# Kernel optimization log

Hardware: AMD Instinct MI355X
Metric: run time of the kernel (lower is better)

Reference implementation:

```python
import jax, jax.numpy as jnp
import numpy as np

B, R, D, H, C = 256, 100, 6168, 128, 100  # batch, replicas, in_dim, hidden, classes


def setup_inputs() -> dict:
    key = jax.random.key(0)
    k1, k2, k3, k4, k5, k6 = jax.random.split(key, 6)
    # binary input features (texas dataset is binary; original casts to bool)
    x = jax.random.randint(k1, (B, D), 0, 2).astype(jnp.int32)
    # Bernoulli(0.5) flip mask, one per replica per feature
    noise = jax.random.randint(k2, (B, R, D), 0, 2).astype(jnp.int32)
    s1 = 1.0 / np.sqrt(D)
    W1 = jax.random.uniform(k3, (D, H), minval=-s1, maxval=s1, dtype=jnp.float32)
    b1 = jax.random.uniform(k4, (H,), minval=-s1, maxval=s1, dtype=jnp.float32)
    s2 = 1.0 / np.sqrt(H)
    W2 = jax.random.uniform(k5, (H, C), minval=-s2, maxval=s2, dtype=jnp.float32)
    b2 = jax.random.uniform(k6, (C,), minval=-s2, maxval=s2, dtype=jnp.float32)
    return {"x": x, "noise": noise, "W1": W1, "b1": b1, "W2": W2, "b2": b2}


def reference(x, noise, W1, b1, W2, b2):
    # np.invert(x, where=noise) on booleans == flip bit where noise==1
    xb = x[:, None, :]                                   # [B,1,D]
    x_noisy = jnp.where(noise == 1, 1 - xb, xb).astype(W1.dtype)  # [B,R,D]
    h = jnp.tanh(jnp.einsum('brd,dh->brh', x_noisy, W1) + b1)      # [B,R,H]
    logits = jnp.einsum('brh,hc->brc', h, W2) + b2                 # [B,R,C]
    return logits.mean(axis=1)                                     # [B,C]
```

## Files before the change

kernel.cpp:

```cpp
#include <hip/hip_runtime.h>
#include <hip/hip_bf16.h>

#define NB 256
#define NR 100
#define NRH 50
#define ND 6168
#define DP 6176
#define NH 128
#define NC 100
#define KSTEP 32
#define NSTEP (DP / KSTEP)
#define MT 64
#define W1T_BYTES ((size_t)NH * DP * 2)

typedef __attribute__((ext_vector_type(8))) __bf16 bf16x8;
typedef __attribute__((ext_vector_type(4))) float f32x4;
typedef __attribute__((ext_vector_type(4))) int i32x4;
typedef __attribute__((ext_vector_type(4))) unsigned int u32x4;

#define BAR() do { asm volatile("s_waitcnt lgkmcnt(0)" ::: "memory"); \
                   __builtin_amdgcn_s_barrier(); } while (0)

__global__ void prep_w1t(const float* __restrict__ W1, __hip_bfloat16* __restrict__ W1T) {
  __shared__ float tile[KSTEP][NH + 1];
  const int d0 = blockIdx.x * KSTEP;
  const int t = threadIdx.x;
#pragma unroll
  for (int p = 0; p < (KSTEP * NH) / 256; ++p) {
    int idx = p * 256 + t;
    int dd = idx >> 7;
    int h  = idx & 127;
    int d  = d0 + dd;
    tile[dd][h] = (d < ND) ? W1[d * NH + h] : 0.f;
  }
  __syncthreads();
#pragma unroll
  for (int p = 0; p < (KSTEP * NH) / 256; ++p) {
    int idx = p * 256 + t;
    int h  = idx >> 5;
    int dd = idx & 31;
    W1T[h * DP + d0 + dd] = __float2bfloat16(tile[dd][h]);
  }
}

__launch_bounds__(256, 2)
__global__ void fused_main(const int* __restrict__ x,
                           const int* __restrict__ noise,
                           const __hip_bfloat16* __restrict__ W1T,
                           const float* __restrict__ b1,
                           float* __restrict__ partials) {
  __shared__ __align__(16) char lds[43072];
  unsigned int* xpair = (unsigned int*)lds;
  char* const BF0 = lds + 12352;
  char* const BF1 = BF0 + 15360;

  const int tid  = threadIdx.x;
  const int lane = tid & 63;
  const int w    = tid >> 6;
  const int lq   = lane >> 4;
  const int lm   = lane & 15;
  const int bid  = blockIdx.x;
  const int b    = bid >> 1;
  const int half = bid & 1;

  const int ar = tid >> 2;
  const int kc = tid & 3;
  const int grow = half * NRH + ((ar < NRH) ? ar : (NRH - 1));
  const int* nrow = noise + (size_t)b * NR * ND + (size_t)grow * ND;

  const int br = tid >> 1;
  const int bh = tid & 1;
  const char* bsrc = (const char*)W1T + (size_t)br * DP * 2 + bh * 32;

  f32x4 acc[4][2] = {};

  auto ISSUE = [&](int s, i32x4* ra, i32x4* rb) {
    i32x4 z = {0, 0, 0, 0};
    const int k0 = s * KSTEP + kc * 8;
    ra[0] = (k0 + 4 <= ND) ? *(const i32x4*)(nrow + k0)     : z;
    ra[1] = (k0 + 8 <= ND) ? *(const i32x4*)(nrow + k0 + 4) : z;
    const long o = (long)s * 64;
    rb[0] = *(const i32x4*)(bsrc + o);
    rb[1] = *(const i32x4*)(bsrc + o + 16);
  };

  auto STORE = [&](int s, const i32x4* ra, const i32x4* rb, char* buf) {
    u32x4 xp = *(const u32x4*)(xpair + s * 16 + kc * 4);
    unsigned pk[4];
#pragma unroll
    for (int p = 0; p < 4; ++p) {
      unsigned n0 = (unsigned)ra[p >> 1][(p & 1) * 2];
      unsigned n1 = (unsigned)ra[p >> 1][(p & 1) * 2 + 1];
      pk[p] = ((n0 | (n1 << 16)) ^ xp[p]) * 0x3F80u;
    }
    u32x4 t = {pk[0], pk[1], pk[2], pk[3]};
    *(u32x4*)(buf + ar * 80 + kc * 16) = t;
    *(i32x4*)(buf + 5120 + br * 80 + bh * 32)      = rb[0];
    *(i32x4*)(buf + 5120 + br * 80 + bh * 32 + 16) = rb[1];
  };

  auto COMPUTE = [&](const char* buf) {
    const char* Bb = buf + 5120;
    bf16x8 bf0 = *(const bf16x8*)(Bb + (w * 32 + lm) * 80 + lq * 16);
    bf16x8 bf1 = *(const bf16x8*)(Bb + (w * 32 + 16 + lm) * 80 + lq * 16);
#pragma unroll
    for (int mf = 0; mf < 4; ++mf) {
      bf16x8 af = *(const bf16x8*)(buf + (mf * 16 + lm) * 80 + lq * 16);
      acc[mf][0] = __builtin_amdgcn_mfma_f32_16x16x32_bf16(af, bf0, acc[mf][0], 0, 0, 0);
      acc[mf][1] = __builtin_amdgcn_mfma_f32_16x16x32_bf16(af, bf1, acc[mf][1], 0, 0, 0);
    }
  };

  i32x4 raA[2], rbA[2], raB[2], rbB[2];

  ISSUE(0, raA, rbA);
  ISSUE(1, raB, rbB);
  {
    const int* xb = x + b * ND;
    for (int i = tid; i < DP / 2; i += 256) {
      unsigned p = 0;
      if (2 * i + 1 < ND) {
        int2 v = *(const int2*)(xb + 2 * i);
        p = ((unsigned)v.x & 1u) | (((unsigned)v.y & 1u) << 16);
      }
      xpair[i] = p;
    }
  }
  BAR();
  STORE(0, raA, rbA, BF0);
  ISSUE(2, raA, rbA);
  BAR();

  for (int s = 0; s < NSTEP; s += 2) {
    COMPUTE(BF0);
    if (s + 1 < NSTEP) STORE(s + 1, raB, rbB, BF1);
    if (s + 3 < NSTEP) ISSUE(s + 3, raB, rbB);
    BAR();
    if (s + 1 < NSTEP) {
      COMPUTE(BF1);
      if (s + 2 < NSTEP) STORE(s + 2, raA, rbA, BF0);
      if (s + 4 < NSTEP) ISSUE(s + 4, raA, rbA);
      BAR();
    }
  }

#pragma unroll
  for (int nf = 0; nf < 2; ++nf) {
    int hcol = w * 32 + nf * 16 + lm;
    float bb = b1[hcol];
    float ssum = 0.f;
#pragma unroll
    for (int mf = 0; mf < 4; ++mf) {
#pragma unroll
      for (int rg = 0; rg < 4; ++rg) {
        int m = mf * 16 + lq * 4 + rg;
        float tv = tanhf(acc[mf][nf][rg] + bb);
        ssum += (m < NRH) ? tv : 0.f;
      }
    }
    ssum += __shfl_xor(ssum, 16, 64);
    ssum += __shfl_xor(ssum, 32, 64);
    if (lq == 0) partials[(size_t)bid * NH + hcol] = ssum;
  }
}

__global__ void combine(const float* __restrict__ partials,
                        const float* __restrict__ W2,
                        const float* __restrict__ b2,
                        float* __restrict__ out) {
  __shared__ float hbar[NH];
  const int b = blockIdx.x;
  const int t = threadIdx.x;
  if (t < NH)
    hbar[t] = (partials[(size_t)(2 * b) * NH + t] + partials[(size_t)(2 * b + 1) * NH + t]) * (1.0f / NR);
  __syncthreads();
  if (t < NC) {
    float s = b2[t];
#pragma unroll 8
    for (int h = 0; h < NH; ++h) s += hbar[h] * W2[h * NC + t];
    out[b * NC + t] = s;
  }
}

extern "C" void kernel_launch(void* const* d_in, const int* in_sizes, int n_in,
                              void* d_out, int out_size, void* d_ws, size_t ws_size,
                              hipStream_t stream) {
  (void)in_sizes; (void)n_in; (void)out_size; (void)ws_size;
  const int* x     = (const int*)d_in[0];
  const int* noise = (const int*)d_in[1];
  const float* W1  = (const float*)d_in[2];
  const float* b1  = (const float*)d_in[3];
  const float* W2  = (const float*)d_in[4];
  const float* b2  = (const float*)d_in[5];
  float* out = (float*)d_out;

  __hip_bfloat16* W1T = (__hip_bfloat16*)d_ws;
  float* partials = (float*)((char*)d_ws + W1T_BYTES);

  prep_w1t<<<DP / KSTEP, 256, 0, stream>>>(W1, W1T);
  fused_main<<<2 * NB, 256, 0, stream>>>(x, noise, W1T, b1, partials);
  combine<<<NB, 128, 0, stream>>>(partials, W2, b2, out);
}
```

Measured before the change: 232.6 us.

## Stream noise directly into LDS via global_load_lds and keep W1 fragments in registers

Replaces the register-staged noise and W1 path with direct global-to-LDS loads (global_load_lds) into a swizzled 128-wide K buffer. W1T fragments now go straight from global memory into registers. The noise XOR and bf16 packing move from the store phase into the compute loop. The goal is to cut VGPR round trips and LDS store traffic on the bandwidth-bound noise stream and to halve barrier count per K. In exchange it uses much larger LDS buffers (78 KB per block), pads D to 6272, and relies on manual vmcnt accounting for correctness.

```diff
diff --git a/kernel.cpp b/kernel.cpp
--- a/kernel.cpp
+++ b/kernel.cpp
@@ -5,28 +5,39 @@
 #define NR 100
 #define NRH 50
 #define ND 6168
-#define DP 6176
+#define DP 6272
 #define NH 128
 #define NC 100
-#define KSTEP 32
-#define NSTEP (DP / KSTEP)
-#define MT 64
+#define NSUP (DP / 128)
 #define W1T_BYTES ((size_t)NH * DP * 2)
 
 typedef __attribute__((ext_vector_type(8))) __bf16 bf16x8;
 typedef __attribute__((ext_vector_type(4))) float f32x4;
 typedef __attribute__((ext_vector_type(4))) int i32x4;
 typedef __attribute__((ext_vector_type(4))) unsigned int u32x4;
-
-#define BAR() do { asm volatile("s_waitcnt lgkmcnt(0)" ::: "memory"); \
-                   __builtin_amdgcn_s_barrier(); } while (0)
+typedef unsigned int u32;
+
+typedef const __attribute__((address_space(1))) u32* gas_ptr;
+typedef __attribute__((address_space(3))) u32* las_ptr;
+
+__device__ __forceinline__ void gload16(const void* g, void* l) {
+  __builtin_amdgcn_global_load_lds((gas_ptr)g, (las_ptr)l, 16, 0, 0);
+}
+
+#define VBAR(N) do { \
+  __builtin_amdgcn_sched_barrier(0); \
+  asm volatile("s_waitcnt vmcnt(" #N ")"); \
+  __builtin_amdgcn_sched_barrier(0); \
+  __builtin_amdgcn_s_barrier(); \
+  __builtin_amdgcn_sched_barrier(0); \
+} while (0)
 
 __global__ void prep_w1t(const float* __restrict__ W1, __hip_bfloat16* __restrict__ W1T) {
-  __shared__ float tile[KSTEP][NH + 1];
-  const int d0 = blockIdx.x * KSTEP;
+  __shared__ float tile[32][NH + 1];
+  const int d0 = blockIdx.x * 32;
   const int t = threadIdx.x;
 #pragma unroll
-  for (int p = 0; p < (KSTEP * NH) / 256; ++p) {
+  for (int p = 0; p < 16; ++p) {
     int idx = p * 256 + t;
     int dd = idx >> 7;
     int h  = idx & 127;
@@ -35,7 +46,7 @@
   }
   __syncthreads();
 #pragma unroll
-  for (int p = 0; p < (KSTEP * NH) / 256; ++p) {
+  for (int p = 0; p < 16; ++p) {
     int idx = p * 256 + t;
     int h  = idx >> 5;
     int dd = idx & 31;
@@ -49,10 +60,10 @@
                            const __hip_bfloat16* __restrict__ W1T,
                            const float* __restrict__ b1,
                            float* __restrict__ partials) {
-  __shared__ __align__(16) char lds[43072];
-  unsigned int* xpair = (unsigned int*)lds;
-  char* const BF0 = lds + 12352;
-  char* const BF1 = BF0 + 15360;
+  __shared__ __align__(16) char lds[78080];
+  u32* xpair = (u32*)lds;
+  char* const A0 = lds + 12544;
+  char* const A1 = A0 + 32768;
 
   const int tid  = threadIdx.x;
   const int lane = tid & 63;
@@ -63,58 +74,61 @@
   const int b    = bid >> 1;
   const int half = bid & 1;
 
-  const int ar = tid >> 2;
-  const int kc = tid & 3;
-  const int grow = half * NRH + ((ar < NRH) ? ar : (NRH - 1));
-  const int* nrow = noise + (size_t)b * NR * ND + (size_t)grow * ND;
-
-  const int br = tid >> 1;
-  const int bh = tid & 1;
-  const char* bsrc = (const char*)W1T + (size_t)br * DP * 2 + bh * 32;
+  const size_t nbase = (size_t)b * NR * ND;
 
   f32x4 acc[4][2] = {};
 
-  auto ISSUE = [&](int s, i32x4* ra, i32x4* rb) {
-    i32x4 z = {0, 0, 0, 0};
-    const int k0 = s * KSTEP + kc * 8;
-    ra[0] = (k0 + 4 <= ND) ? *(const i32x4*)(nrow + k0)     : z;
-    ra[1] = (k0 + 8 <= ND) ? *(const i32x4*)(nrow + k0 + 4) : z;
-    const long o = (long)s * 64;
-    rb[0] = *(const i32x4*)(bsrc + o);
-    rb[1] = *(const i32x4*)(bsrc + o + 16);
+  struct Bregs { bf16x8 f[8]; };
+  Bregs B0r, B1r;
+
+  auto STAGE = [&](int s, char* dst) {
+#pragma unroll
+    for (int i = 0; i < 8; ++i) {
+      const int call = w * 8 + i;
+      const int row  = call * 2 + (lane >> 5);
+      const int gr   = half * NRH + ((row < NRH) ? row : (NRH - 1));
+      const int slot = lane & 31;
+      const int slotp = slot ^ (row & 7);
+      int kint = s * 128 + slotp * 4;
+      kint = (kint + 4 <= ND) ? kint : 0;
+      gload16(noise + nbase + (size_t)gr * ND + kint, dst + call * 1024);
+    }
   };
 
-  auto STORE = [&](int s, const i32x4* ra, const i32x4* rb, char* buf) {
-    u32x4 xp = *(const u32x4*)(xpair + s * 16 + kc * 4);
-    unsigned pk[4];
-#pragma unroll
-    for (int p = 0; p < 4; ++p) {
-      unsigned n0 = (unsigned)ra[p >> 1][(p & 1) * 2];
-      unsigned n1 = (unsigned)ra[p >> 1][(p & 1) * 2 + 1];
-      pk[p] = ((n0 | (n1 << 16)) ^ xp[p]) * 0x3F80u;
-    }
-    u32x4 t = {pk[0], pk[1], pk[2], pk[3]};
-    *(u32x4*)(buf + ar * 80 + kc * 16) = t;
-    *(i32x4*)(buf + 5120 + br * 80 + bh * 32)      = rb[0];
-    *(i32x4*)(buf + 5120 + br * 80 + bh * 32 + 16) = rb[1];
+  auto BLOAD = [&](int s, Bregs& Br) {
+#pragma unroll
+    for (int kt = 0; kt < 4; ++kt)
+#pragma unroll
+      for (int nf = 0; nf < 2; ++nf)
+        Br.f[kt * 2 + nf] = *(const bf16x8*)(W1T + (size_t)(w * 32 + nf * 16 + lm) * DP
+                                             + s * 128 + kt * 32 + lq * 8);
   };
 
-  auto COMPUTE = [&](const char* buf) {
-    const char* Bb = buf + 5120;
-    bf16x8 bf0 = *(const bf16x8*)(Bb + (w * 32 + lm) * 80 + lq * 16);
-    bf16x8 bf1 = *(const bf16x8*)(Bb + (w * 32 + 16 + lm) * 80 + lq * 16);
-#pragma unroll
-    for (int mf = 0; mf < 4; ++mf) {
-      bf16x8 af = *(const bf16x8*)(buf + (mf * 16 + lm) * 80 + lq * 16);
-      acc[mf][0] = __builtin_amdgcn_mfma_f32_16x16x32_bf16(af, bf0, acc[mf][0], 0, 0, 0);
-      acc[mf][1] = __builtin_amdgcn_mfma_f32_16x16x32_bf16(af, bf1, acc[mf][1], 0, 0, 0);
+  auto COMPUTE = [&](int s, const char* Ab, const Bregs& Br) {
+#pragma unroll
+    for (int kt = 0; kt < 4; ++kt) {
+      u32x4 xp = *(const u32x4*)(xpair + s * 64 + kt * 16 + lq * 4);
+#pragma unroll
+      for (int mf = 0; mf < 4; ++mf) {
+        const int row = mf * 16 + lm;
+        const int s0  = kt * 8 + lq * 2;
+        const char* base = Ab + row * 512;
+        i32x4 v0 = *(const i32x4*)(base + ((s0    ) ^ (row & 7)) * 16);
+        i32x4 v1 = *(const i32x4*)(base + ((s0 + 1) ^ (row & 7)) * 16);
+        u32 pk0 = (((u32)v0[0] | ((u32)v0[1] << 16)) ^ xp[0]) * 0x3F80u;
+        u32 pk1 = (((u32)v0[2] | ((u32)v0[3] << 16)) ^ xp[1]) * 0x3F80u;
+        u32 pk2 = (((u32)v1[0] | ((u32)v1[1] << 16)) ^ xp[2]) * 0x3F80u;
+        u32 pk3 = (((u32)v1[2] | ((u32)v1[3] << 16)) ^ xp[3]) * 0x3F80u;
+        u32x4 pkv = {pk0, pk1, pk2, pk3};
+        bf16x8 af = *(bf16x8*)&pkv;
+        acc[mf][0] = __builtin_amdgcn_mfma_f32_16x16x32_bf16(af, Br.f[kt * 2 + 0], acc[mf][0], 0, 0, 0);
+        acc[mf][1] = __builtin_amdgcn_mfma_f32_16x16x32_bf16(af, Br.f[kt * 2 + 1], acc[mf][1], 0, 0, 0);
+      }
     }
   };
 
-  i32x4 raA[2], rbA[2], raB[2], rbB[2];
-
-  ISSUE(0, raA, rbA);
-  ISSUE(1, raB, rbB);
+  STAGE(0, A0);
+  BLOAD(0, B0r);
   {
     const int* xb = x + b * ND;
     for (int i = tid; i < DP / 2; i += 256) {
@@ -126,23 +140,20 @@
       xpair[i] = p;
     }
   }
-  BAR();
-  STORE(0, raA, rbA, BF0);
-  ISSUE(2, raA, rbA);
-  BAR();
-
-  for (int s = 0; s < NSTEP; s += 2) {
-    COMPUTE(BF0);
-    if (s + 1 < NSTEP) STORE(s + 1, raB, rbB, BF1);
-    if (s + 3 < NSTEP) ISSUE(s + 3, raB, rbB);
-    BAR();
-    if (s + 1 < NSTEP) {
-      COMPUTE(BF1);
-      if (s + 2 < NSTEP) STORE(s + 2, raA, rbA, BF0);
-      if (s + 4 < NSTEP) ISSUE(s + 4, raA, rbA);
-      BAR();
-    }
-  }
+  __syncthreads();
+
+  for (int s = 0; s < NSUP - 1; s += 2) {
+    VBAR(8);
+    STAGE(s + 1, A1);
+    BLOAD(s + 1, B1r);
+    COMPUTE(s, A0, B0r);
+
+    VBAR(8);
+    if (s + 2 < NSUP) { STAGE(s + 2, A0); BLOAD(s + 2, B0r); }
+    COMPUTE(s + 1, A1, B1r);
+  }
+  VBAR(8);
+  COMPUTE(NSUP - 1, A0, B0r);
 
 #pragma unroll
   for (int nf = 0; nf < 2; ++nf) {
@@ -197,7 +208,7 @@
   __hip_bfloat16* W1T = (__hip_bfloat16*)d_ws;
   float* partials = (float*)((char*)d_ws + W1T_BYTES);
 
-  prep_w1t<<<DP / KSTEP, 256, 0, stream>>>(W1, W1T);
+  prep_w1t<<<DP / 32, 256, 0, stream>>>(W1, W1T);
   fused_main<<<2 * NB, 256, 0, stream>>>(x, noise, W1T, b1, partials);
   combine<<<NB, 128, 0, stream>>>(partials, W2, b2, out);
 }
```

Result: faster. 211.9 us (-8.9%).
